# Performance work log

Hardware: AMD Instinct MI355X
Metric: run time of the kernel (lower is better)

## Reference

```python
import jax, jax.numpy as jnp
import numpy as np

B, T, C, NH = 1, 2048, 1024, 16
HS = C // NH            # 64
LEVEL = 6
LMIN = 2 ** LEVEL       # 64 (tail block size)
NB = T // LMIN          # 32 complete sets


def setup_inputs() -> dict:
    key = jax.random.key(0)
    ks = jax.random.split(key, 8)
    def w(k, shape, fan_in):
        return jax.random.normal(k, shape, jnp.float32) / np.sqrt(fan_in)
    return {
        "x": jax.random.normal(ks[0], (B, T, C), jnp.float32),
        "Wq": w(ks[1], (C, C), C),
        "Wk": w(ks[2], (C, C), C),
        "Wv": w(ks[3], (C, C), C),
        "Wkmap": w(ks[4], (HS, HS * HS), HS * HS),
        "bkmap": jnp.zeros((HS,), jnp.float32),
        "Wvmap": w(ks[5], (HS, HS * HS), HS * HS),
        "bvmap": jnp.zeros((HS,), jnp.float32),
        "Wc": w(ks[6], (C, C), C),
        "bc": jnp.zeros((C,), jnp.float32),
    }


def reference(x, Wq, Wk, Wv, Wkmap, bkmap, Wvmap, bvmap, Wc, bc):
    phi = lambda t: jax.nn.elu(t) + 1.0  # feature_map='elu'
    # preprocess: projections + feature map (no q/k normalization)
    q = phi((x @ Wq.T).reshape(B, T, NH, HS))
    k = phi((x @ Wk.T).reshape(B, T, NH, HS))
    v = (x @ Wv.T).reshape(B, T, NH, HS)

    # per-position outer products k_t (x) v_t, grouped into LMIN-sized blocks
    op = jnp.einsum('bthd,bthe->bthde', k, v).reshape(B, NB, LMIN, NH, HS, HS)
    # set feature = final state of linear-attn recurrence over each full block
    set_f = op.sum(axis=2).reshape(B, NB, NH, HS * HS)            # [B,NB,NH,HS^2]
    # tail feature at t = state over [t - t%LMIN, t] = in-block prefix cumsum
    tail_f = jnp.cumsum(op, axis=2).reshape(B, T, NH, HS * HS)    # [B,T,NH,HS^2]

    K = set_f @ Wkmap.T + bkmap      # [B,NB,NH,HS] (k_mapping=True)
    V = set_f @ Wvmap.T + bvmap      # [B,NB,NH,HS] (v_mapping=True)
    K_tail = tail_f @ Wkmap.T + bkmap  # [B,T,NH,HS]
    V_tail = tail_f @ Wvmap.T + bvmap  # [B,T,NH,HS]

    scale = 1.0 / np.sqrt(HS)
    logits = jnp.einsum('bthd,bshd->bhts', q, K) * scale          # [B,NH,T,NB]
    # query t may attend only complete sets strictly before its own block
    mask = jnp.arange(NB)[None, :] < (jnp.arange(T) // LMIN)[:, None]  # [T,NB]
    logits = jnp.where(mask[None, None], logits, -jnp.inf)
    tail_logit = (jnp.einsum('bthd,bthd->bth', q, K_tail) * scale)
    tail_logit = tail_logit.transpose(0, 2, 1)[..., None]         # [B,NH,T,1]

    att = jax.nn.softmax(jnp.concatenate([logits, tail_logit], axis=-1), axis=-1)
    out = (jnp.einsum('bhts,bshd->bhtd', att[..., :-1], V)
           + att[..., -1:] * V_tail.transpose(0, 2, 1, 3))        # [B,NH,T,HS]
    out = out.transpose(0, 2, 1, 3).reshape(B, T, C)
    return out @ Wc.T + bc
```

## Files before the change

### kernel.cpp

```cpp
#include <hip/hip_runtime.h>
#include <hip/hip_bf16.h>
#include <math.h>

typedef __hip_bfloat16 bf16;
typedef __attribute__((ext_vector_type(8))) short short8;
typedef __attribute__((ext_vector_type(4))) float f32x4;

#define C_DIM 1024
#define NHEAD 16
#define HS 64

__device__ __forceinline__ float bf2f(bf16 x) { return __bfloat162float(x); }
__device__ __forceinline__ short bfbits(float x) {
    bf16 h = __float2bfloat16(x);
    return *reinterpret_cast<short*>(&h);
}

__device__ __forceinline__ void gl16(const void* g, void* l) {
    __builtin_amdgcn_global_load_lds(
        (const __attribute__((address_space(1))) unsigned int*)g,
        (__attribute__((address_space(3))) unsigned int*)l, 16, 0, 0);
}

__device__ __forceinline__ void split8(const float* p, short8& h, short8& l) {
    float4 f0 = reinterpret_cast<const float4*>(p)[0];
    float4 f1 = reinterpret_cast<const float4*>(p)[1];
    float vals[8] = {f0.x, f0.y, f0.z, f0.w, f1.x, f1.y, f1.z, f1.w};
#pragma unroll
    for (int j = 0; j < 8; ++j) {
        bf16 hb = __float2bfloat16(vals[j]);
        float r = vals[j] - __bfloat162float(hb);
        h[j] = *reinterpret_cast<short*>(&hb);
        bf16 lb = __float2bfloat16(r);
        l[j] = *reinterpret_cast<short*>(&lb);
    }
}

__device__ __forceinline__ short8* tchunk(bf16* tile, int row, int ch) {
    return reinterpret_cast<short8*>(tile + row * 64 + (((ch) ^ (row & 7)) << 3));
}

__global__ __launch_bounds__(256) void presplit_all_kernel(
    const float* __restrict__ x, const float* __restrict__ Wq,
    const float* __restrict__ Wk, const float* __restrict__ Wv,
    bf16* __restrict__ xh, bf16* __restrict__ xl,
    bf16* __restrict__ wqh, bf16* __restrict__ wql,
    bf16* __restrict__ wkh, bf16* __restrict__ wkl,
    bf16* __restrict__ wvh, bf16* __restrict__ wvl)
{
    int blk = blockIdx.x;
    const float* src; bf16 *dh, *dl; long off;
    if (blk < 1024)      { src = x;  dh = xh;  dl = xl;  off = (long)blk * 2048; }
    else if (blk < 1536) { src = Wq; dh = wqh; dl = wql; off = (long)(blk - 1024) * 2048; }
    else if (blk < 2048) { src = Wk; dh = wkh; dl = wkl; off = (long)(blk - 1536) * 2048; }
    else                 { src = Wv; dh = wvh; dl = wvl; off = (long)(blk - 2048) * 2048; }
    long p = off + threadIdx.x * 8;
    int j = (int)(((p >> 3) ^ (p >> 10)) & 7);
    long dp = (p & ~56l) | ((long)j << 3);
    short8 h8, l8;
    split8(&src[p], h8, l8);
    *reinterpret_cast<short8*>(&dh[dp]) = h8;
    *reinterpret_cast<short8*>(&dl[dp]) = l8;
}

__global__ __launch_bounds__(256) void presplit_wc_kernel(
    const float* __restrict__ Wc, bf16* __restrict__ wch, bf16* __restrict__ wcl)
{
    long p = (long)blockIdx.x * 2048 + threadIdx.x * 8;
    int j = (int)(((p >> 3) ^ (p >> 10)) & 7);
    long dp = (p & ~56l) | ((long)j << 3);
    short8 h8, l8;
    split8(&Wc[p], h8, l8);
    *reinterpret_cast<short8*>(&wch[dp]) = h8;
    *reinterpret_cast<short8*>(&wcl[dp]) = l8;
}

__global__ __launch_bounds__(256) void presplit_wmap_kernel(
    const float* __restrict__ WK, const float* __restrict__ WV, bf16* __restrict__ Wm4)
{
    int d = blockIdx.x;
    int row = threadIdx.x >> 2, e0 = (threadIdx.x & 3) * 16;
    int sw0 = (((e0 >> 3) + 0) ^ (row & 7)) & 7;
    int sw1 = (((e0 >> 3) + 1) ^ (row & 7)) & 7;
    const float* pk = &WK[(long)row * 4096 + d * 64 + e0];
    const float* pv = &WV[(long)row * 4096 + d * 64 + e0];
    long bKh = ((long)(d * 4 + 0) * 64 + row) * 64;
    long bKl = ((long)(d * 4 + 1) * 64 + row) * 64;
    long bVh = ((long)(d * 4 + 2) * 64 + row) * 64;
    long bVl = ((long)(d * 4 + 3) * 64 + row) * 64;
    short8 h8, l8;
    split8(pk, h8, l8);     *(short8*)&Wm4[bKh + sw0*8] = h8; *(short8*)&Wm4[bKl + sw0*8] = l8;
    split8(pk + 8, h8, l8); *(short8*)&Wm4[bKh + sw1*8] = h8; *(short8*)&Wm4[bKl + sw1*8] = l8;
    split8(pv, h8, l8);     *(short8*)&Wm4[bVh + sw0*8] = h8; *(short8*)&Wm4[bVl + sw0*8] = l8;
    split8(pv + 8, h8, l8); *(short8*)&Wm4[bVh + sw1*8] = h8; *(short8*)&Wm4[bVl + sw1*8] = l8;
}

__global__ __launch_bounds__(256) void qkv_kernel(
    const bf16* __restrict__ xh, const bf16* __restrict__ xl,
    const bf16* __restrict__ wqh, const bf16* __restrict__ wql,
    const bf16* __restrict__ wkh, const bf16* __restrict__ wkl,
    const bf16* __restrict__ wvh, const bf16* __restrict__ wvl,
    float* __restrict__ qkv, float* __restrict__ kTg)
{
    __shared__ bf16 lds[32768];
    const int tid = threadIdx.x;
    const int lane = tid & 63, wid = tid >> 6;
    const int wr = wid >> 1, wc = wid & 1;
    const int proj = blockIdx.x >> 3;
    const int n0 = (blockIdx.x & 7) * 128;
    const int m0 = blockIdx.y * 128;
    const bf16* Bhp = proj == 0 ? wqh : (proj == 1 ? wkh : wvh);
    const bf16* Blp = proj == 0 ? wql : (proj == 1 ? wkl : wvl);
    float* C = qkv + (long)proj * 2097152;
    char* lb = reinterpret_cast<char*>(lds);

    f32x4 acc[4][4] = {};
    for (int kt = 0; kt < 16; ++kt) {
        const int k0 = kt << 6;
#pragma unroll
        for (int i = 0; i < 4; ++i) {
            int cc = tid + i * 256;
            int row = cc >> 3, j = cc & 7;
            long soA = (long)(m0 + row) * 1024 + k0 + j * 8;
            long soB = (long)(n0 + row) * 1024 + k0 + j * 8;
            gl16(&xh[soA],  lb + cc * 16);
            gl16(&xl[soA],  lb + 16384 + cc * 16);
            gl16(&Bhp[soB], lb + 32768 + cc * 16);
            gl16(&Blp[soB], lb + 49152 + cc * 16);
        }
        __syncthreads();
#pragma unroll
        for (int kk = 0; kk < 2; ++kk) {
            short8 afh[4], afl[4], bfh[4], bfl[4];
#pragma unroll
            for (int t = 0; t < 4; ++t) {
                int ra = wr * 64 + t * 16 + (lane & 15);
                int rb = wc * 64 + t * 16 + (lane & 15);
                int ch = kk * 4 + (lane >> 4);
                afh[t] = *tchunk(lds, ra, ch);
                afl[t] = *tchunk(lds + 8192, ra, ch);
                bfh[t] = *tchunk(lds + 16384, rb, ch);
                bfl[t] = *tchunk(lds + 24576, rb, ch);
            }
#pragma unroll
            for (int tm = 0; tm < 4; ++tm)
#pragma unroll
                for (int tn = 0; tn < 4; ++tn) {
                    acc[tm][tn] = __builtin_amdgcn_mfma_f32_16x16x32_bf16(
                        afh[tm], bfh[tn], acc[tm][tn], 0, 0, 0);
                    acc[tm][tn] = __builtin_amdgcn_mfma_f32_16x16x32_bf16(
                        afh[tm], bfl[tn], acc[tm][tn], 0, 0, 0);
                    acc[tm][tn] = __builtin_amdgcn_mfma_f32_16x16x32_bf16(
                        afl[tm], bfh[tn], acc[tm][tn], 0, 0, 0);
                }
        }
        __syncthreads();
    }
    if (proj == 1) {
        float* lf = reinterpret_cast<float*>(lds) + wid * 4096;
#pragma unroll
        for (int tm = 0; tm < 4; ++tm)
#pragma unroll
            for (int tn = 0; tn < 4; ++tn)
#pragma unroll
                for (int r = 0; r < 4; ++r) {
                    int s = tm * 16 + (lane >> 4) * 4 + r;
                    int dd = tn * 16 + (lane & 15);
                    float v = acc[tm][tn][r];
                    v = v > 0.f ? v + 1.f : __expf(v);
                    lf[dd * 64 + (s ^ dd)] = v;
                }
        asm volatile("s_waitcnt lgkmcnt(0)" ::: "memory");
        __builtin_amdgcn_sched_barrier(0);
        int pair = (blockIdx.y * 2 + wr) * 16 + ((blockIdx.x & 7) * 2 + wc);
        long pb = (long)pair * 4096;
        int s0 = (lane & 15) * 4;
#pragma unroll
        for (int ii = 0; ii < 16; ++ii) {
            int dd = (lane >> 4) * 16 + ii;
            float4 o;
            o.x = lf[dd * 64 + ((s0 + 0) ^ dd)];
            o.y = lf[dd * 64 + ((s0 + 1) ^ dd)];
            o.z = lf[dd * 64 + ((s0 + 2) ^ dd)];
            o.w = lf[dd * 64 + ((s0 + 3) ^ dd)];
            *reinterpret_cast<float4*>(&kTg[pb + (long)dd * 64 + s0]) = o;
        }
    } else {
#pragma unroll
        for (int tm = 0; tm < 4; ++tm)
#pragma unroll
            for (int tn = 0; tn < 4; ++tn)
#pragma unroll
                for (int r = 0; r < 4; ++r) {
                    int row = m0 + wr * 64 + tm * 16 + (lane >> 4) * 4 + r;
                    int col = n0 + wc * 64 + tn * 16 + (lane & 15);
                    float v = acc[tm][tn][r];
                    if (proj == 0) v = v > 0.f ? v + 1.f : __expf(v);
                    C[(long)row * 1024 + col] = v;
                }
    }
}

__global__ __launch_bounds__(512, 4) void setfeat_kernel(
    const float* __restrict__ kTg, const float* __restrict__ vbuf,
    const bf16* __restrict__ Wm4,
    const float* __restrict__ bkmap, const float* __restrict__ bvmap,
    float* __restrict__ Ktail, float* __restrict__ Vtail,
    float* __restrict__ KsetT, float* __restrict__ Vset)
{
    __shared__ char smem[32768];
    bf16* W0 = reinterpret_cast<bf16*>(smem);
    bf16* W1 = reinterpret_cast<bf16*>(smem + 16384);
    const int tid = threadIdx.x;
    const int side = blockIdx.x & 1;
    const int grp = tid >> 8, tl = tid & 255;
    const int lane = tl & 63, wid = tl >> 6;
    const int wr = wid >> 1, wc = wid & 1;
    const int pairIdx = (blockIdx.x >> 1) * 2 + grp;
    const int b = pairIdx >> 4, h = pairIdx & 15;
    const long base_kv = ((long)b * 64) * C_DIM + h * HS;
    const float* kp = kTg + (long)pairIdx * 4096;
    const long wsideoff = (long)side * 8192;

    short8 vh[2][2];
#pragma unroll
    for (int tm = 0; tm < 2; ++tm)
#pragma unroll
        for (int kk = 0; kk < 2; ++kk) {
            const float* vp = &vbuf[base_kv +
                (long)(wr * 32 + tm * 16 + (lane & 15)) * C_DIM + kk * 32 + (lane >> 4) * 8];
            float4 f0 = reinterpret_cast<const float4*>(vp)[0];
            float4 f1 = reinterpret_cast<const float4*>(vp)[1];
            float vals[8] = {f0.x, f0.y, f0.z, f0.w, f1.x, f1.y, f1.z, f1.w};
#pragma unroll
            for (int j = 0; j < 8; ++j) vh[tm][kk][j] = bfbits(vals[j]);
        }
    f32x4 kvc[2];
#pragma unroll
    for (int tm = 0; tm < 2; ++tm)
        kvc[tm] = *reinterpret_cast<const f32x4*>(
            &kp[wr * 32 + tm * 16 + (lane >> 4) * 4]);
#pragma unroll
    for (int i = 0; i < 2; ++i) {
        int cc = tid + i * 512;
        gl16(&Wm4[wsideoff + (long)cc * 8], smem + (long)cc * 16);
    }
    f32x4 acc[2][2] = {};
    __syncthreads();

    for (int d = 0; d < 64; ++d) {
        bf16* Wcur = (d & 1) ? W1 : W0;
        char* Wnxt = (d & 1) ? smem : smem + 16384;
        __builtin_amdgcn_s_barrier();
        f32x4 kvn[2] = {};
        if (d < 63) {
#pragma unroll
            for (int i = 0; i < 2; ++i) {
                int cc = tid + i * 512;
                gl16(&Wm4[(long)(d + 1) * 16384 + wsideoff + (long)cc * 8],
                     Wnxt + (long)cc * 16);
            }
#pragma unroll
            for (int tm = 0; tm < 2; ++tm)
                kvn[tm] = *reinterpret_cast<const f32x4*>(
                    &kp[(d + 1) * 64 + wr * 32 + tm * 16 + (lane >> 4) * 4]);
            asm volatile("s_waitcnt vmcnt(4)" ::: "memory");
        } else {
            asm volatile("s_waitcnt vmcnt(0)" ::: "memory");
        }
        f32x4 G[2][2] = {};
#pragma unroll
        for (int kk = 0; kk < 2; ++kk) {
            short8 bh_[2], bl_[2];
#pragma unroll
            for (int t = 0; t < 2; ++t) {
                int rb = wc * 32 + t * 16 + (lane & 15);
                int ch = kk * 4 + (lane >> 4);
                bh_[t] = *tchunk(Wcur,        rb, ch);
                bl_[t] = *tchunk(Wcur + 4096, rb, ch);
            }
#pragma unroll
            for (int tm = 0; tm < 2; ++tm)
#pragma unroll
                for (int tn = 0; tn < 2; ++tn) {
                    G[tm][tn] = __builtin_amdgcn_mfma_f32_16x16x32_bf16(
                        vh[tm][kk], bh_[tn], G[tm][tn], 0, 0, 0);
                    G[tm][tn] = __builtin_amdgcn_mfma_f32_16x16x32_bf16(
                        vh[tm][kk], bl_[tn], G[tm][tn], 0, 0, 0);
                }
        }
#pragma unroll
        for (int tm = 0; tm < 2; ++tm)
#pragma unroll
            for (int tn = 0; tn < 2; ++tn)
#pragma unroll
                for (int r = 0; r < 4; ++r)
                    acc[tm][tn][r] += kvc[tm][r] * G[tm][tn][r];
        kvc[0] = kvn[0]; kvc[1] = kvn[1];
    }
    __syncthreads();
    float(*Wall)[64] = reinterpret_cast<float(*)[64]>(smem + grp * 16384);
#pragma unroll
    for (int tm = 0; tm < 2; ++tm)
#pragma unroll
        for (int tn = 0; tn < 2; ++tn)
#pragma unroll
            for (int r = 0; r < 4; ++r) {
                int row = wr * 32 + tm * 16 + (lane >> 4) * 4 + r;
                int col = wc * 32 + tn * 16 + (lane & 15);
                Wall[row][col] = acc[tm][tn][r];
            }
    __syncthreads();
    if (tl < 64) {
        int i = tl;
        const float bi = side ? bvmap[i] : bkmap[i];
        float run = 0.f;
        for (int s = 0; s < 64; ++s) {
            run += Wall[s][i];
            float val = run + bi;
            long t = (long)b * 64 + s;
            if (side) Vtail[t * C_DIM + h * HS + i] = val;
            else      Ktail[t * C_DIM + h * HS + i] = val;
            if (s == 63) {
                if (side) Vset[(b * NHEAD + h) * HS + i] = val;
                else      KsetT[h * 2048 + i * 32 + b] = val;
            }
        }
    }
}

__global__ __launch_bounds__(256) void attn_kernel(
    const float* __restrict__ qbuf, const float* __restrict__ KsetT,
    const float* __restrict__ Vset, const float* __restrict__ Ktail,
    const float* __restrict__ Vtail, bf16* __restrict__ atth, bf16* __restrict__ attl)
{
    __shared__ float qsh[4][64];
    __shared__ float attsh[4][64];
    const int tid = threadIdx.x, lane = tid & 63, wid = tid >> 6;
    const int g = blockIdx.x * 4 + wid;
    const int t = g >> 4, h = g & 15;
    const int nb = t >> 6;
    const float scale = 0.125f;
    const long qoff = (long)t * C_DIM + h * HS;
    float qv = qbuf[qoff + lane];
    qsh[wid][lane] = qv;
    float tp = qv * Ktail[qoff + lane];
    for (int off = 32; off; off >>= 1) tp += __shfl_xor(tp, off, 64);
    __syncthreads();
    float logit = -INFINITY;
    if (lane < nb) {
        float s = 0.f;
        const float* Kp = &KsetT[h * 2048 + lane];
        for (int d = 0; d < 64; ++d) s += qsh[wid][d] * Kp[d * 32];
        logit = s * scale;
    } else if (lane == nb) {
        logit = tp * scale;
    }
    float m = logit;
    for (int off = 32; off; off >>= 1) m = fmaxf(m, __shfl_xor(m, off, 64));
    float e = (lane <= nb) ? __expf(logit - m) : 0.f;
    float sum = e;
    for (int off = 32; off; off >>= 1) sum += __shfl_xor(sum, off, 64);
    attsh[wid][lane] = e / sum;
    __syncthreads();
    float out = 0.f;
    for (int s = 0; s < nb; ++s)
        out += attsh[wid][s] * Vset[(s * NHEAD + h) * HS + lane];
    out += attsh[wid][nb] * Vtail[qoff + lane];
    bf16 hb = __float2bfloat16(out);
    int csw = (((lane >> 3) ^ (t & 7)) << 3) | (lane & 7);
    long po = (long)t * 1024 + h * 64 + csw;
    atth[po] = hb;
    attl[po] = __float2bfloat16(out - bf2f(hb));
}

__global__ __launch_bounds__(256) void gemm_final_kernel(
    const bf16* __restrict__ ah, const bf16* __restrict__ al,
    const bf16* __restrict__ bh, const bf16* __restrict__ bl,
    const float* __restrict__ bias, float* __restrict__ C)
{
    __shared__ bf16 lds[24576];
    const int tid = threadIdx.x;
    const int lane = tid & 63, wid = tid >> 6;
    const int wr = wid >> 1, wc = wid & 1;
    const int m0 = blockIdx.y * 128, n0 = blockIdx.x * 64;
    char* lb = reinterpret_cast<char*>(lds);

    f32x4 acc[4][2] = {};
    for (int kt = 0; kt < 16; ++kt) {
        const int k0 = kt << 6;
#pragma unroll
        for (int i = 0; i < 4; ++i) {
            int cc = tid + i * 256;
            int row = cc >> 3, j = cc & 7;
            long so = (long)(m0 + row) * 1024 + k0 + j * 8;
            gl16(&ah[so], lb + cc * 16);
            gl16(&al[so], lb + 16384 + cc * 16);
        }
#pragma unroll
        for (int i = 0; i < 2; ++i) {
            int cc = tid + i * 256;
            int row = cc >> 3, j = cc & 7;
            long so = (long)(n0 + row) * 1024 + k0 + j * 8;
            gl16(&bh[so], lb + 32768 + cc * 16);
            gl16(&bl[so], lb + 40960 + cc * 16);
        }
        __syncthreads();
#pragma unroll
        for (int kk = 0; kk < 2; ++kk) {
            short8 afh[4], afl[4], bfh[2], bfl[2];
#pragma unroll
            for (int t = 0; t < 4; ++t) {
                int ra = wr * 64 + t * 16 + (lane & 15);
                int ch = kk * 4 + (lane >> 4);
                afh[t] = *tchunk(lds, ra, ch);
                afl[t] = *tchunk(lds + 8192, ra, ch);
            }
#pragma unroll
            for (int t = 0; t < 2; ++t) {
                int rb = wc * 32 + t * 16 + (lane & 15);
                int ch = kk * 4 + (lane >> 4);
                bfh[t] = *tchunk(lds + 16384, rb, ch);
                bfl[t] = *tchunk(lds + 20480, rb, ch);
            }
#pragma unroll
            for (int tm = 0; tm < 4; ++tm)
#pragma unroll
                for (int tn = 0; tn < 2; ++tn) {
                    acc[tm][tn] = __builtin_amdgcn_mfma_f32_16x16x32_bf16(
                        afh[tm], bfh[tn], acc[tm][tn], 0, 0, 0);
                    acc[tm][tn] = __builtin_amdgcn_mfma_f32_16x16x32_bf16(
                        afh[tm], bfl[tn], acc[tm][tn], 0, 0, 0);
                    acc[tm][tn] = __builtin_amdgcn_mfma_f32_16x16x32_bf16(
                        afl[tm], bfh[tn], acc[tm][tn], 0, 0, 0);
                }
        }
        __syncthreads();
    }
#pragma unroll
    for (int tm = 0; tm < 4; ++tm)
#pragma unroll
        for (int tn = 0; tn < 2; ++tn)
#pragma unroll
            for (int r = 0; r < 4; ++r) {
                int row = m0 + wr * 64 + tm * 16 + (lane >> 4) * 4 + r;
                int col = n0 + wc * 32 + tn * 16 + (lane & 15);
                C[(long)row * 1024 + col] = acc[tm][tn][r] + bias[col];
            }
}

extern "C" void kernel_launch(void* const* d_in, const int* in_sizes, int n_in,
                              void* d_out, int out_size, void* d_ws, size_t ws_size,
                              hipStream_t stream)
{
    const float* x     = (const float*)d_in[0];
    const float* Wq    = (const float*)d_in[1];
    const float* Wk    = (const float*)d_in[2];
    const float* Wv    = (const float*)d_in[3];
    const float* Wkmap = (const float*)d_in[4];
    const float* bkmap = (const float*)d_in[5];
    const float* Wvmap = (const float*)d_in[6];
    const float* bvmap = (const float*)d_in[7];
    const float* Wc    = (const float*)d_in[8];
    const float* bc    = (const float*)d_in[9];
    float* out = (float*)d_out;

    char* ws = (char*)d_ws;
    const long MB = 1l << 20;
    float* q   = (float*)(ws + 0 * MB);
    float* kTg = (float*)(ws + 8 * MB);
    float* v   = (float*)(ws + 16 * MB);
    bf16* xh   = (bf16*)(ws + 24 * MB);
    bf16* xl   = (bf16*)(ws + 28 * MB);
    bf16* wqh  = (bf16*)(ws + 32 * MB);
    bf16* wql  = (bf16*)(ws + 34 * MB);
    bf16* wkh  = (bf16*)(ws + 36 * MB);
    bf16* wkl  = (bf16*)(ws + 38 * MB);
    bf16* wvh  = (bf16*)(ws + 40 * MB);
    bf16* wvl  = (bf16*)(ws + 42 * MB);
    bf16* Wm4  = (bf16*)(ws + 44 * MB);
    float* Ktail = (float*)(ws + 24 * MB);
    float* Vtail = (float*)(ws + 32 * MB);
    float* KsetT = (float*)(ws + 40 * MB);
    float* Vset  = (float*)(ws + 41 * MB);
    bf16* atth   = (bf16*)(ws + 8 * MB);
    bf16* attl   = (bf16*)(ws + 12 * MB);
    bf16* wch    = (bf16*)(ws + 44 * MB);
    bf16* wcl    = (bf16*)(ws + 46 * MB);

    presplit_all_kernel<<<2560, 256, 0, stream>>>(x, Wq, Wk, Wv, xh, xl,
                                                  wqh, wql, wkh, wkl, wvh, wvl);
    presplit_wmap_kernel<<<64, 256, 0, stream>>>(Wkmap, Wvmap, Wm4);
    qkv_kernel<<<dim3(24, 16), 256, 0, stream>>>(xh, xl, wqh, wql, wkh, wkl,
                                                 wvh, wvl, q, kTg);
    setfeat_kernel<<<512, 512, 0, stream>>>(kTg, v, Wm4, bkmap, bvmap,
                                            Ktail, Vtail, KsetT, Vset);
    presplit_wc_kernel<<<512, 256, 0, stream>>>(Wc, wch, wcl);
    attn_kernel<<<8192, 256, 0, stream>>>(q, KsetT, Vset, Ktail, Vtail, atth, attl);
    gemm_final_kernel<<<dim3(16, 16), 256, 0, stream>>>(atth, attl, wch, wcl, bc, out);
}
```

Baseline: 253.3 us.

## Fuse presplit kernels into neighbours and triple-buffer setfeat weight loads

Folds the Wkmap/Wvmap presplit into presplit_all_kernel and the Wc presplit into attn_kernel as extra blocks, removing two kernel launches. In setfeat_kernel, the double-buffered LDS weight stream becomes a three-stage ring (48KB) that prefetches two iterations ahead, with vmcnt waits adjusted to match. The occupancy hint goes to 6, which may conflict with the larger LDS footprint and limit residency. The extra Wc blocks in attn_kernel also add tail work to that kernel.

```diff
diff --git a/kernel.cpp b/kernel.cpp
--- a/kernel.cpp
+++ b/kernel.cpp
@@ -43,12 +43,32 @@
 __global__ __launch_bounds__(256) void presplit_all_kernel(
     const float* __restrict__ x, const float* __restrict__ Wq,
     const float* __restrict__ Wk, const float* __restrict__ Wv,
+    const float* __restrict__ WK, const float* __restrict__ WV,
     bf16* __restrict__ xh, bf16* __restrict__ xl,
     bf16* __restrict__ wqh, bf16* __restrict__ wql,
     bf16* __restrict__ wkh, bf16* __restrict__ wkl,
-    bf16* __restrict__ wvh, bf16* __restrict__ wvl)
+    bf16* __restrict__ wvh, bf16* __restrict__ wvl,
+    bf16* __restrict__ Wm4)
 {
     int blk = blockIdx.x;
+    if (blk >= 2560) {
+        int d = blk - 2560;
+        int row = threadIdx.x >> 2, e0 = (threadIdx.x & 3) * 16;
+        int sw0 = (((e0 >> 3) + 0) ^ (row & 7)) & 7;
+        int sw1 = (((e0 >> 3) + 1) ^ (row & 7)) & 7;
+        const float* pk = &WK[(long)row * 4096 + d * 64 + e0];
+        const float* pv = &WV[(long)row * 4096 + d * 64 + e0];
+        long bKh = ((long)(d * 4 + 0) * 64 + row) * 64;
+        long bKl = ((long)(d * 4 + 1) * 64 + row) * 64;
+        long bVh = ((long)(d * 4 + 2) * 64 + row) * 64;
+        long bVl = ((long)(d * 4 + 3) * 64 + row) * 64;
+        short8 h8, l8;
+        split8(pk, h8, l8);     *(short8*)&Wm4[bKh + sw0*8] = h8; *(short8*)&Wm4[bKl + sw0*8] = l8;
+        split8(pk + 8, h8, l8); *(short8*)&Wm4[bKh + sw1*8] = h8; *(short8*)&Wm4[bKl + sw1*8] = l8;
+        split8(pv, h8, l8);     *(short8*)&Wm4[bVh + sw0*8] = h8; *(short8*)&Wm4[bVl + sw0*8] = l8;
+        split8(pv + 8, h8, l8); *(short8*)&Wm4[bVh + sw1*8] = h8; *(short8*)&Wm4[bVl + sw1*8] = l8;
+        return;
+    }
     const float* src; bf16 *dh, *dl; long off;
     if (blk < 1024)      { src = x;  dh = xh;  dl = xl;  off = (long)blk * 2048; }
     else if (blk < 1536) { src = Wq; dh = wqh; dl = wql; off = (long)(blk - 1024) * 2048; }
@@ -61,38 +81,6 @@
     split8(&src[p], h8, l8);
     *reinterpret_cast<short8*>(&dh[dp]) = h8;
     *reinterpret_cast<short8*>(&dl[dp]) = l8;
-}
-
-__global__ __launch_bounds__(256) void presplit_wc_kernel(
-    const float* __restrict__ Wc, bf16* __restrict__ wch, bf16* __restrict__ wcl)
-{
-    long p = (long)blockIdx.x * 2048 + threadIdx.x * 8;
-    int j = (int)(((p >> 3) ^ (p >> 10)) & 7);
-    long dp = (p & ~56l) | ((long)j << 3);
-    short8 h8, l8;
-    split8(&Wc[p], h8, l8);
-    *reinterpret_cast<short8*>(&wch[dp]) = h8;
-    *reinterpret_cast<short8*>(&wcl[dp]) = l8;
-}
-
-__global__ __launch_bounds__(256) void presplit_wmap_kernel(
-    const float* __restrict__ WK, const float* __restrict__ WV, bf16* __restrict__ Wm4)
-{
-    int d = blockIdx.x;
-    int row = threadIdx.x >> 2, e0 = (threadIdx.x & 3) * 16;
-    int sw0 = (((e0 >> 3) + 0) ^ (row & 7)) & 7;
-    int sw1 = (((e0 >> 3) + 1) ^ (row & 7)) & 7;
-    const float* pk = &WK[(long)row * 4096 + d * 64 + e0];
-    const float* pv = &WV[(long)row * 4096 + d * 64 + e0];
-    long bKh = ((long)(d * 4 + 0) * 64 + row) * 64;
-    long bKl = ((long)(d * 4 + 1) * 64 + row) * 64;
-    long bVh = ((long)(d * 4 + 2) * 64 + row) * 64;
-    long bVl = ((long)(d * 4 + 3) * 64 + row) * 64;
-    short8 h8, l8;
-    split8(pk, h8, l8);     *(short8*)&Wm4[bKh + sw0*8] = h8; *(short8*)&Wm4[bKl + sw0*8] = l8;
-    split8(pk + 8, h8, l8); *(short8*)&Wm4[bKh + sw1*8] = h8; *(short8*)&Wm4[bKl + sw1*8] = l8;
-    split8(pv, h8, l8);     *(short8*)&Wm4[bVh + sw0*8] = h8; *(short8*)&Wm4[bVl + sw0*8] = l8;
-    split8(pv + 8, h8, l8); *(short8*)&Wm4[bVh + sw1*8] = h8; *(short8*)&Wm4[bVl + sw1*8] = l8;
 }
 
 __global__ __launch_bounds__(256) void qkv_kernel(
@@ -201,16 +189,14 @@
     }
 }
 
-__global__ __launch_bounds__(512, 4) void setfeat_kernel(
+__global__ __launch_bounds__(512, 6) void setfeat_kernel(
     const float* __restrict__ kTg, const float* __restrict__ vbuf,
     const bf16* __restrict__ Wm4,
     const float* __restrict__ bkmap, const float* __restrict__ bvmap,
     float* __restrict__ Ktail, float* __restrict__ Vtail,
     float* __restrict__ KsetT, float* __restrict__ Vset)
 {
-    __shared__ char smem[32768];
-    bf16* W0 = reinterpret_cast<bf16*>(smem);
-    bf16* W1 = reinterpret_cast<bf16*>(smem + 16384);
+    __shared__ char smem[49152];
     const int tid = threadIdx.x;
     const int side = blockIdx.x & 1;
     const int grp = tid >> 8, tl = tid & 255;
@@ -235,35 +221,44 @@
 #pragma unroll
             for (int j = 0; j < 8; ++j) vh[tm][kk][j] = bfbits(vals[j]);
         }
+#pragma unroll
+    for (int i = 0; i < 2; ++i) {
+        int cc = tid + i * 512;
+        gl16(&Wm4[wsideoff + (long)cc * 8], smem + (long)cc * 16);
+    }
+#pragma unroll
+    for (int i = 0; i < 2; ++i) {
+        int cc = tid + i * 512;
+        gl16(&Wm4[16384 + wsideoff + (long)cc * 8], smem + 16384 + (long)cc * 16);
+    }
     f32x4 kvc[2];
 #pragma unroll
     for (int tm = 0; tm < 2; ++tm)
         kvc[tm] = *reinterpret_cast<const f32x4*>(
             &kp[wr * 32 + tm * 16 + (lane >> 4) * 4]);
-#pragma unroll
-    for (int i = 0; i < 2; ++i) {
-        int cc = tid + i * 512;
-        gl16(&Wm4[wsideoff + (long)cc * 8], smem + (long)cc * 16);
-    }
     f32x4 acc[2][2] = {};
     __syncthreads();
 
     for (int d = 0; d < 64; ++d) {
-        bf16* Wcur = (d & 1) ? W1 : W0;
-        char* Wnxt = (d & 1) ? smem : smem + 16384;
+        bf16* Wcur = reinterpret_cast<bf16*>(smem + (d % 3) * 16384);
         __builtin_amdgcn_s_barrier();
         f32x4 kvn[2] = {};
         if (d < 63) {
 #pragma unroll
-            for (int i = 0; i < 2; ++i) {
-                int cc = tid + i * 512;
-                gl16(&Wm4[(long)(d + 1) * 16384 + wsideoff + (long)cc * 8],
-                     Wnxt + (long)cc * 16);
-            }
-#pragma unroll
             for (int tm = 0; tm < 2; ++tm)
                 kvn[tm] = *reinterpret_cast<const f32x4*>(
                     &kp[(d + 1) * 64 + wr * 32 + tm * 16 + (lane >> 4) * 4]);
+        }
+        if (d < 62) {
+            char* Wnxt = smem + ((d + 2) % 3) * 16384;
+#pragma unroll
+            for (int i = 0; i < 2; ++i) {
+                int cc = tid + i * 512;
+                gl16(&Wm4[(long)(d + 2) * 16384 + wsideoff + (long)cc * 8],
+                     Wnxt + (long)cc * 16);
+            }
+            asm volatile("s_waitcnt vmcnt(6)" ::: "memory");
+        } else if (d == 62) {
             asm volatile("s_waitcnt vmcnt(4)" ::: "memory");
         } else {
             asm volatile("s_waitcnt vmcnt(0)" ::: "memory");
@@ -332,11 +327,23 @@
 __global__ __launch_bounds__(256) void attn_kernel(
     const float* __restrict__ qbuf, const float* __restrict__ KsetT,
     const float* __restrict__ Vset, const float* __restrict__ Ktail,
-    const float* __restrict__ Vtail, bf16* __restrict__ atth, bf16* __restrict__ attl)
+    const float* __restrict__ Vtail, bf16* __restrict__ atth, bf16* __restrict__ attl,
+    const float* __restrict__ Wc, bf16* __restrict__ wch, bf16* __restrict__ wcl)
 {
     __shared__ float qsh[4][64];
     __shared__ float attsh[4][64];
-    const int tid = threadIdx.x, lane = tid & 63, wid = tid >> 6;
+    const int tid = threadIdx.x;
+    if (blockIdx.x >= 8192) {
+        long p = (long)(blockIdx.x - 8192) * 2048 + tid * 8;
+        int j = (int)(((p >> 3) ^ (p >> 10)) & 7);
+        long dp = (p & ~56l) | ((long)j << 3);
+        short8 h8, l8;
+        split8(&Wc[p], h8, l8);
+        *reinterpret_cast<short8*>(&wch[dp]) = h8;
+        *reinterpret_cast<short8*>(&wcl[dp]) = l8;
+        return;
+    }
+    const int lane = tid & 63, wid = tid >> 6;
     const int g = blockIdx.x * 4 + wid;
     const int t = g >> 4, h = g & 15;
     const int nb = t >> 6;
@@ -488,14 +495,14 @@
     bf16* wch    = (bf16*)(ws + 44 * MB);
     bf16* wcl    = (bf16*)(ws + 46 * MB);
 
-    presplit_all_kernel<<<2560, 256, 0, stream>>>(x, Wq, Wk, Wv, xh, xl,
-                                                  wqh, wql, wkh, wkl, wvh, wvl);
-    presplit_wmap_kernel<<<64, 256, 0, stream>>>(Wkmap, Wvmap, Wm4);
+    presplit_all_kernel<<<2624, 256, 0, stream>>>(x, Wq, Wk, Wv, Wkmap, Wvmap,
+                                                  xh, xl, wqh, wql, wkh, wkl,
+                                                  wvh, wvl, Wm4);
     qkv_kernel<<<dim3(24, 16), 256, 0, stream>>>(xh, xl, wqh, wql, wkh, wkl,
                                                  wvh, wvl, q, kTg);
     setfeat_kernel<<<512, 512, 0, stream>>>(kTg, v, Wm4, bkmap, bvmap,
                                             Ktail, Vtail, KsetT, Vset);
-    presplit_wc_kernel<<<512, 256, 0, stream>>>(Wc, wch, wcl);
-    attn_kernel<<<8192, 256, 0, stream>>>(q, KsetT, Vset, Ktail, Vtail, atth, attl);
+    attn_kernel<<<8704, 256, 0, stream>>>(q, KsetT, Vset, Ktail, Vtail, atth, attl,
+                                          Wc, wch, wcl);
     gemm_final_kernel<<<dim3(16, 16), 256, 0, stream>>>(atth, attl, wch, wcl, bc, out);
 }
```

Result: slower. 310.4 us (+22.5%).
